# Kernel optimization log

Hardware: AMD Instinct MI355X
Metric: run time of the kernel (lower is better)

## Reference

```python
import jax, jax.numpy as jnp
import numpy as np

B, T, D, H = 2, 2048, 2048, 16
HD = D // H  # 128


def _rope_tables(t, hd):
    # standard RoPE frequencies
    inv_freq = 1.0 / (10000.0 ** (np.arange(0, hd, 2, dtype=np.float32) / hd))
    pos = np.arange(t, dtype=np.float32)
    freqs = np.outer(pos, inv_freq)          # [t, hd/2]
    emb = np.concatenate([freqs, freqs], -1)  # [t, hd]
    return jnp.asarray(np.cos(emb)), jnp.asarray(np.sin(emb))


def setup_inputs() -> dict:
    key = jax.random.key(0)
    k1, k2, k3 = jax.random.split(key, 3)
    x = jax.random.normal(k1, (B, T, D), dtype=jnp.float32)
    cos, sin = _rope_tables(T, HD)
    Wqkv = jax.random.normal(k2, (3 * D, D), dtype=jnp.float32) * (D ** -0.5)
    Wout = jax.random.normal(k3, (D, D), dtype=jnp.float32) * (D ** -0.5)
    return {"x": x, "cos": cos, "sin": sin, "Wqkv": Wqkv, "Wout": Wout}


def _rotate_half(u):
    u1, u2 = jnp.split(u, 2, axis=-1)
    return jnp.concatenate([-u2, u1], axis=-1)


def _apply_rotary(u, cos, sin):
    # u: [b,h,t,hd]; cos/sin: [t,hd] broadcast over b,h
    return u * cos[None, None] + _rotate_half(u) * sin[None, None]


def reference(x, cos, sin, Wqkv, Wout):
    b, t, d = x.shape
    qkv = jnp.einsum('btd,ed->bte', x, Wqkv)                 # [b,t,3d]
    qkv = qkv.reshape(b, t, 3, H, HD).transpose(2, 0, 3, 1, 4)  # [3,b,h,t,hd]
    q, k, v = qkv[0], qkv[1], qkv[2]
    q = _apply_rotary(q, cos, sin)
    k = _apply_rotary(k, cos, sin)
    scale = 1.0 / jnp.sqrt(jnp.asarray(HD, dtype=x.dtype))
    scores = jnp.einsum('bhqe,bhke->bhqk', q, k) * scale      # [b,h,t,t]
    causal = jnp.tril(jnp.ones((t, t), dtype=bool))
    scores = jnp.where(causal[None, None], scores, jnp.asarray(-jnp.inf, dtype=scores.dtype))
    probs = jax.nn.softmax(scores, axis=-1)
    attn = jnp.einsum('bhqk,bhke->bhqe', probs, v)            # [b,h,t,hd]
    attn = attn.transpose(0, 2, 1, 3).reshape(b, t, d)
    return jnp.einsum('btd,ed->bte', attn, Wout)
```

## Files before the change

### kernel.cpp

```cpp
#include <hip/hip_runtime.h>
#include <hip/hip_bf16.h>
#include <stdint.h>

#define T_SEQ 2048
#define D_MODEL 2048
#define N_HEADS 16
#define HEAD_DIM 128

typedef __hip_bfloat16 bf16_t;
typedef __attribute__((ext_vector_type(8))) short short8;
typedef __attribute__((ext_vector_type(4))) short short4v;
typedef __attribute__((ext_vector_type(4))) float f32x4;

__device__ __forceinline__ unsigned short f2bf(float x) {
  union { float f; unsigned u; } c; c.f = x;
  unsigned u = c.u;
  u += 0x7fffu + ((u >> 16) & 1u);
  return (unsigned short)(u >> 16);
}
__device__ __forceinline__ float bf2f(short v) {
  union { unsigned u; float f; } c;
  c.u = ((unsigned)(unsigned short)v) << 16;
  return c.f;
}
__device__ __forceinline__ void async16(const bf16_t* g, bf16_t* l) {
  __builtin_amdgcn_global_load_lds(
      (const __attribute__((address_space(1))) void*)g,
      (__attribute__((address_space(3))) void*)l, 16, 0, 0);
}

__global__ __launch_bounds__(256) void cvt_kernel(const float* __restrict__ in,
                                                  unsigned short* __restrict__ out,
                                                  int n4) {
  int i = blockIdx.x * 256 + threadIdx.x;
  if (i >= n4) return;
  float4 v = ((const float4*)in)[i];
  short4v o;
  o[0] = (short)f2bf(v.x); o[1] = (short)f2bf(v.y);
  o[2] = (short)f2bf(v.z); o[3] = (short)f2bf(v.w);
  ((short4v*)out)[i] = o;
}

template<int F32OUT>
__global__ __launch_bounds__(512, 4) void gemm_tp_kernel(
    const bf16_t* __restrict__ A, const bf16_t* __restrict__ Bm,
    float* __restrict__ Cf, unsigned short* __restrict__ Cb,
    int M, int N, int K, int nbn) {
  __shared__ bf16_t lds[36864];
  const int tid = threadIdx.x;
  const int w = tid >> 6, lane = tid & 63;
  const int wm = w >> 2, wn = w & 3;
  const int l15 = lane & 15, g = lane >> 4;

  const int nwg = gridDim.x;
  const int cpx = nwg >> 3;
  const int wg = (blockIdx.x & 7) * cpx + (blockIdx.x >> 3);
  const int bm0 = (wg / nbn) * 128, bn0 = (wg % nbn) * 256;

  const int sl = tid >> 3;
  const int su = (tid & 7) ^ (sl & 7);
  const int srow = (sl << 1) | (su >> 2);
  const int sc8 = su & 3;
  const bf16_t* agA = A + (size_t)(bm0 + srow) * K + sc8 * 8;
  const bf16_t* agB = Bm + (size_t)(bn0 + srow) * K + sc8 * 8;

#define STAGE(KT, SB) do {                                                    \
    bf16_t* _d = lds + (SB) * 12288 + w * 512;         \
    async16(agA + (size_t)(KT) * 32, _d);                                     \
    async16(agB + (size_t)(KT) * 32, _d + 4096);                              \
    async16(agB + 128 * (size_t)K + (size_t)(KT) * 32, _d + 8192);            \
  } while (0)

  const int lhalf = l15 >> 1;
  const int aoff = lhalf * 64 + (((((l15 & 1) << 2) | g) ^ lhalf)) * 8;
  const bf16_t* Abase = lds + wm * 2048 + aoff;
  const bf16_t* Bbase = lds + 4096 + wn * 2048 + aoff;

  f32x4 acc[4][4];
#pragma unroll
  for (int i = 0; i < 4; ++i)
#pragma unroll
    for (int j = 0; j < 4; ++j)
#pragma unroll
      for (int e = 0; e < 4; ++e) acc[i][j][e] = 0.0f;

  STAGE(0, 0);
  STAGE(1, 1);

  const int NT = K >> 5;
  int cb = 0, sb = 2;
  for (int kt = 0; kt < NT - 1; ++kt) {
    asm volatile("s_waitcnt vmcnt(3)" ::: "memory");
    __builtin_amdgcn_s_barrier();
    const bf16_t* Ab = Abase + cb * 12288;
    const bf16_t* Bb = Bbase + cb * 12288;
    short8 af[4], bfr[4];
#pragma unroll
    for (int mi = 0; mi < 4; ++mi) af[mi] = *(const short8*)(Ab + mi * 512);
#pragma unroll
    for (int ni = 0; ni < 4; ++ni) bfr[ni] = *(const short8*)(Bb + ni * 512);
    if (kt < NT - 2) STAGE(kt + 2, sb);
    __builtin_amdgcn_s_setprio(1);
#pragma unroll
    for (int mi = 0; mi < 4; ++mi)
#pragma unroll
      for (int ni = 0; ni < 4; ++ni)
        acc[mi][ni] = __builtin_amdgcn_mfma_f32_16x16x32_bf16(
            af[mi], bfr[ni], acc[mi][ni], 0, 0, 0);
    __builtin_amdgcn_s_setprio(0);
    cb = (cb == 2) ? 0 : cb + 1;
    sb = (sb == 2) ? 0 : sb + 1;
  }
  {
    asm volatile("s_waitcnt vmcnt(0)" ::: "memory");
    __builtin_amdgcn_s_barrier();
    const bf16_t* Ab = Abase + cb * 12288;
    const bf16_t* Bb = Bbase + cb * 12288;
    short8 af[4], bfr[4];
#pragma unroll
    for (int mi = 0; mi < 4; ++mi) af[mi] = *(const short8*)(Ab + mi * 512);
#pragma unroll
    for (int ni = 0; ni < 4; ++ni) bfr[ni] = *(const short8*)(Bb + ni * 512);
    __builtin_amdgcn_s_setprio(1);
#pragma unroll
    for (int mi = 0; mi < 4; ++mi)
#pragma unroll
      for (int ni = 0; ni < 4; ++ni)
        acc[mi][ni] = __builtin_amdgcn_mfma_f32_16x16x32_bf16(
            af[mi], bfr[ni], acc[mi][ni], 0, 0, 0);
    __builtin_amdgcn_s_setprio(0);
  }
#undef STAGE

#pragma unroll
  for (int mi = 0; mi < 4; ++mi)
#pragma unroll
    for (int ni = 0; ni < 4; ++ni)
#pragma unroll
      for (int r = 0; r < 4; ++r) {
        int mr = bm0 + wm * 64 + mi * 16 + g * 4 + r;
        int nc = bn0 + wn * 64 + ni * 16 + l15;
        if (F32OUT)
          Cf[(size_t)mr * N + nc] = acc[mi][ni][r];
        else
          Cb[(size_t)mr * N + nc] = f2bf(acc[mi][ni][r]);
      }
}

__global__ __launch_bounds__(256) void rope_kernel(
    const bf16_t* __restrict__ qkv,
    const float* __restrict__ cosb, const float* __restrict__ sinb,
    bf16_t* __restrict__ qo, bf16_t* __restrict__ ko, bf16_t* __restrict__ vT) {
  const int nTT = T_SEQ / 64;
  const int bx = blockIdx.x;
  const int bh = bx / nTT, tt = bx % nTT;
  const int b = bh / N_HEADS, h = bh % N_HEADS;
  const int tid = threadIdx.x;
  __shared__ bf16_t vlds[64][136];

  const float SC = 0.08838834764831845f;

#pragma unroll
  for (int it = 0; it < 2; ++it) {
    int item = it * 256 + tid;
    int r = item >> 3, cg = item & 7;
    int t = tt * 64 + r;
    int c0 = cg * 8;
    size_t base = ((size_t)b * T_SEQ + t) * (size_t)(3 * D_MODEL) + (size_t)h * HEAD_DIM;

    float cs0[8], sn0[8], cs1[8], sn1[8];
    {
      const float* cp = cosb + (size_t)t * HEAD_DIM + c0;
      const float* sp = sinb + (size_t)t * HEAD_DIM + c0;
      float4 a0 = *(const float4*)(cp), a1 = *(const float4*)(cp + 4);
      float4 b0 = *(const float4*)(cp + 64), b1 = *(const float4*)(cp + 68);
      float4 s0 = *(const float4*)(sp), s1 = *(const float4*)(sp + 4);
      float4 t0 = *(const float4*)(sp + 64), t1 = *(const float4*)(sp + 68);
      cs0[0]=a0.x; cs0[1]=a0.y; cs0[2]=a0.z; cs0[3]=a0.w; cs0[4]=a1.x; cs0[5]=a1.y; cs0[6]=a1.z; cs0[7]=a1.w;
      cs1[0]=b0.x; cs1[1]=b0.y; cs1[2]=b0.z; cs1[3]=b0.w; cs1[4]=b1.x; cs1[5]=b1.y; cs1[6]=b1.z; cs1[7]=b1.w;
      sn0[0]=s0.x; sn0[1]=s0.y; sn0[2]=s0.z; sn0[3]=s0.w; sn0[4]=s1.x; sn0[5]=s1.y; sn0[6]=s1.z; sn0[7]=s1.w;
      sn1[0]=t0.x; sn1[1]=t0.y; sn1[2]=t0.z; sn1[3]=t0.w; sn1[4]=t1.x; sn1[5]=t1.y; sn1[6]=t1.z; sn1[7]=t1.w;
    }

#pragma unroll
    for (int sec = 0; sec < 2; ++sec) {
      size_t sbase = base + (size_t)sec * D_MODEL;
      short8 lo = *(const short8*)(qkv + sbase + c0);
      short8 hi = *(const short8*)(qkv + sbase + 64 + c0);
      short8 olo, ohi;
#pragma unroll
      for (int e = 0; e < 8; ++e) {
        float xl = bf2f(lo[e]), xh = bf2f(hi[e]);
        float rl = xl * cs0[e] - xh * sn0[e];
        float rh = xh * cs1[e] + xl * sn1[e];
        if (sec == 0) { rl *= SC; rh *= SC; }
        olo[e] = (short)f2bf(rl);
        ohi[e] = (short)f2bf(rh);
      }
      bf16_t* dst = (sec == 0 ? qo : ko) + ((size_t)bh * T_SEQ + t) * HEAD_DIM + c0;
      *(short8*)dst = olo;
      *(short8*)(dst + 64) = ohi;
    }

    short8 v0 = *(const short8*)(qkv + base + 2 * D_MODEL + c0);
    short8 v1 = *(const short8*)(qkv + base + 2 * D_MODEL + 64 + c0);
    *(short8*)&vlds[r][c0] = v0;
    *(short8*)&vlds[r][64 + c0] = v1;
  }
  __syncthreads();

  int hd = tid >> 1, hf = tid & 1;
  bf16_t* dst = vT + ((size_t)bh * HEAD_DIM + hd) * T_SEQ + tt * 64 + hf * 32;
#pragma unroll
  for (int jj = 0; jj < 4; ++jj) {
    short8 o;
#pragma unroll
    for (int e = 0; e < 8; ++e)
      o[e] = *(const short*)&vlds[hf * 32 + jj * 8 + e][hd];
    *(short8*)(dst + jj * 8) = o;
  }
}

__global__ __launch_bounds__(256) void attn_kernel(
    const bf16_t* __restrict__ q, const bf16_t* __restrict__ k,
    const bf16_t* __restrict__ vT, unsigned short* __restrict__ attn) {
  const int bx = blockIdx.x;
  const int bh = bx & 31;
  const int qt = 31 - (bx >> 5);
  const int b = bh / N_HEADS, h = bh % N_HEADS;
  const int tid = threadIdx.x;
  const int w = tid >> 6, lane = tid & 63;
  const int l15 = lane & 15, g = lane >> 4;
  const float LOG2E = 1.44269504088896340736f;

  __shared__ bf16_t Ks[2][64 * 128];
  __shared__ bf16_t Vs[2][128 * 64];
  __shared__ bf16_t plds[4][16][72];

  const bf16_t* qb = q + (size_t)bh * T_SEQ * HEAD_DIM;
  const bf16_t* kb = k + (size_t)bh * T_SEQ * HEAD_DIM;
  const bf16_t* vb = vT + (size_t)bh * HEAD_DIM * T_SEQ;

  const int qrow = qt * 64 + w * 16 + l15;
  short8 qf[4];
#pragma unroll
  for (int kk = 0; kk < 4; ++kk)
    qf[kk] = *(const short8*)(qb + (size_t)qrow * HEAD_DIM + kk * 32 + g * 8);

  float m[4], l[4];
  f32x4 acc[8];
#pragma unroll
  for (int r = 0; r < 4; ++r) { m[r] = -3.0e38f; l[r] = 0.0f; }
#pragma unroll
  for (int fh = 0; fh < 8; ++fh)
#pragma unroll
    for (int e = 0; e < 4; ++e) acc[fh][e] = 0.0f;

#define STAGE_TILES(KT, BU)                                                      \
  {                                                                              \
    _Pragma("unroll")                                                            \
    for (int j = 0; j < 4; ++j) {                                                \
      int s = j * 4 + w;                                                         \
      int row = s * 4 + (lane >> 4);                                             \
      int gc = (lane & 15) ^ (row & 7);                                          \
      async16(kb + (size_t)((KT) * 64 + row) * HEAD_DIM + gc * 8,                \
              &Ks[BU][s * 512]);                                                 \
    }                                                                            \
    _Pragma("unroll")                                                            \
    for (int j = 0; j < 4; ++j) {                                                \
      int s = j * 4 + w;                                                         \
      int row = s * 8 + (lane >> 3);                                             \
      int gc = (lane & 7) ^ (row & 7);                                           \
      async16(vb + (size_t)row * T_SEQ + (KT) * 64 + gc * 8,                     \
              &Vs[BU][s * 512]);                                                 \
    }                                                                            \
  }

  STAGE_TILES(0, 0);
  __syncthreads();
  int buf = 0;

  for (int kt = 0; kt <= qt; ++kt) {
    if (kt < qt) STAGE_TILES(kt + 1, buf ^ 1);

    f32x4 s[4];
#pragma unroll
    for (int f = 0; f < 4; ++f)
#pragma unroll
      for (int e = 0; e < 4; ++e) s[f][e] = 0.0f;
    __builtin_amdgcn_s_setprio(1);
#pragma unroll
    for (int f = 0; f < 4; ++f) {
      int row = f * 16 + l15;
      int r7 = l15 & 7;
#pragma unroll
      for (int kk = 0; kk < 4; ++kk) {
        short8 kf = *(const short8*)(&Ks[buf][row * 128 + (((kk * 4 + g) ^ r7) << 3)]);
        s[f] = __builtin_amdgcn_mfma_f32_16x16x32_bf16(qf[kk], kf, s[f], 0, 0, 0);
      }
    }
    __builtin_amdgcn_s_setprio(0);

    if (kt == qt) {
#pragma unroll
      for (int f = 0; f < 4; ++f) {
        int kv = f * 16 + l15;
#pragma unroll
        for (int r = 0; r < 4; ++r) {
          int qq = w * 16 + g * 4 + r;
          if (kv > qq) s[f][r] = -3.0e38f;
        }
      }
    }
    float rmax[4];
#pragma unroll
    for (int r = 0; r < 4; ++r)
      rmax[r] = fmaxf(fmaxf(s[0][r], s[1][r]), fmaxf(s[2][r], s[3][r]));
#pragma unroll
    for (int off = 1; off < 16; off <<= 1)
#pragma unroll
      for (int r = 0; r < 4; ++r)
        rmax[r] = fmaxf(rmax[r], __shfl_xor(rmax[r], off, 64));

    float fac[4], rsum[4];
#pragma unroll
    for (int r = 0; r < 4; ++r) {
      float mn = fmaxf(m[r], rmax[r]);
      fac[r] = exp2f((m[r] - mn) * LOG2E);
      m[r] = mn;
      rsum[r] = 0.0f;
    }
#pragma unroll
    for (int f = 0; f < 4; ++f)
#pragma unroll
      for (int r = 0; r < 4; ++r) {
        float pv = exp2f((s[f][r] - m[r]) * LOG2E);
        s[f][r] = pv;
        rsum[r] += pv;
      }
#pragma unroll
    for (int off = 1; off < 16; off <<= 1)
#pragma unroll
      for (int r = 0; r < 4; ++r)
        rsum[r] += __shfl_xor(rsum[r], off, 64);
#pragma unroll
    for (int r = 0; r < 4; ++r) l[r] = l[r] * fac[r] + rsum[r];
#pragma unroll
    for (int fh = 0; fh < 8; ++fh)
#pragma unroll
      for (int r = 0; r < 4; ++r) acc[fh][r] *= fac[r];

#pragma unroll
    for (int f = 0; f < 4; ++f)
#pragma unroll
      for (int r = 0; r < 4; ++r)
        *(unsigned short*)&plds[w][g * 4 + r][f * 16 + l15] = f2bf(s[f][r]);

    short8 pf0 = *(const short8*)&plds[w][l15][g * 8];
    short8 pf1 = *(const short8*)&plds[w][l15][32 + g * 8];

    __builtin_amdgcn_s_setprio(1);
#pragma unroll
    for (int fh = 0; fh < 8; ++fh) {
      int row = fh * 16 + l15;
      int r7 = l15 & 7;
      short8 vf0 = *(const short8*)(&Vs[buf][row * 64 + ((g ^ r7) << 3)]);
      short8 vf1 = *(const short8*)(&Vs[buf][row * 64 + (((4 + g) ^ r7) << 3)]);
      acc[fh] = __builtin_amdgcn_mfma_f32_16x16x32_bf16(pf0, vf0, acc[fh], 0, 0, 0);
      acc[fh] = __builtin_amdgcn_mfma_f32_16x16x32_bf16(pf1, vf1, acc[fh], 0, 0, 0);
    }
    __builtin_amdgcn_s_setprio(0);

    __syncthreads();
    buf ^= 1;
  }

  float inv[4];
#pragma unroll
  for (int r = 0; r < 4; ++r) inv[r] = 1.0f / l[r];
#pragma unroll
  for (int fh = 0; fh < 8; ++fh)
#pragma unroll
    for (int r = 0; r < 4; ++r) {
      int tg = qt * 64 + w * 16 + g * 4 + r;
      attn[((size_t)b * T_SEQ + tg) * D_MODEL + (size_t)h * HEAD_DIM + fh * 16 + l15] =
          f2bf(acc[fh][r] * inv[r]);
    }
}

extern "C" void kernel_launch(void* const* d_in, const int* in_sizes, int n_in,
                              void* d_out, int out_size, void* d_ws, size_t ws_size,
                              hipStream_t stream) {
  const float* x    = (const float*)d_in[0];
  const float* cosb = (const float*)d_in[1];
  const float* sinb = (const float*)d_in[2];
  const float* Wqkv = (const float*)d_in[3];
  const float* Wout = (const float*)d_in[4];
  float* out = (float*)d_out;

  char* ws = (char*)d_ws;
  size_t off = 0;
  bf16_t* xb    = (bf16_t*)(ws + off); off += (size_t)4096 * 2048 * 2;
  bf16_t* wqkvb = (bf16_t*)(ws + off); off += (size_t)6144 * 2048 * 2;
  bf16_t* woutb = (bf16_t*)(ws + off); off += (size_t)2048 * 2048 * 2;
  bf16_t* qkvb  = (bf16_t*)(ws + off); off += (size_t)4096 * 6144 * 2;
  bf16_t* qb    = (bf16_t*)(ws + off); off += (size_t)32 * 2048 * 128 * 2;
  bf16_t* kb    = (bf16_t*)(ws + off); off += (size_t)32 * 2048 * 128 * 2;
  bf16_t* vTb   = (bf16_t*)(ws + off); off += (size_t)32 * 2048 * 128 * 2;
  bf16_t* attnb = xb;

  cvt_kernel<<<8192, 256, 0, stream>>>(x, (unsigned short*)xb, 4096 * 2048 / 4);
  cvt_kernel<<<12288, 256, 0, stream>>>(Wqkv, (unsigned short*)wqkvb, 6144 * 2048 / 4);
  cvt_kernel<<<4096, 256, 0, stream>>>(Wout, (unsigned short*)woutb, 2048 * 2048 / 4);

  gemm_tp_kernel<0><<<768, 512, 0, stream>>>(xb, wqkvb, nullptr, (unsigned short*)qkvb,
                                             4096, 6144, 2048, 24);

  rope_kernel<<<1024, 256, 0, stream>>>(qkvb, cosb, sinb, qb, kb, vTb);

  attn_kernel<<<1024, 256, 0, stream>>>(qb, kb, vTb, (unsigned short*)attnb);

  gemm_tp_kernel<1><<<256, 512, 0, stream>>>(attnb, woutb, out, nullptr,
                                             4096, 2048, 2048, 8);
}
```

Baseline: 297.7 us.

## Software-pipeline attention loop: overlap next QK^T with current softmax and PV

Restructures the flash-attention inner loop so K and V tiles are staged separately. The QK^T MFMAs for the next tile are issued before the softmax and PV of the current tile, with explicit vmcnt waits and raw s_barriers in place of __syncthreads. The goal is to hide softmax and exp latency behind matrix work and to load K one tile ahead of V. This adds register pressure from the second score buffer, and the hand-tuned waitcnt counts must exactly match the number of outstanding async loads.

```diff
diff --git a/kernel.cpp b/kernel.cpp
--- a/kernel.cpp
+++ b/kernel.cpp
@@ -65,7 +65,7 @@
   const bf16_t* agB = Bm + (size_t)(bn0 + srow) * K + sc8 * 8;
 
 #define STAGE(KT, SB) do {                                                    \
-    bf16_t* _d = lds + (SB) * 12288 + w * 512;         \
+    bf16_t* _d = lds + (SB) * 12288 + w * 512;                                \
     async16(agA + (size_t)(KT) * 32, _d);                                     \
     async16(agB + (size_t)(KT) * 32, _d + 4096);                              \
     async16(agB + 128 * (size_t)K + (size_t)(KT) * 32, _d + 8192);            \
@@ -256,8 +256,10 @@
 #pragma unroll
     for (int e = 0; e < 4; ++e) acc[fh][e] = 0.0f;
 
-#define STAGE_TILES(KT, BU)                                                      \
-  {                                                                              \
+  f32x4 SA[4], SB[4];
+  const int r7 = l15 & 7;
+
+#define STAGE_K(KT, BU) {                                                        \
     _Pragma("unroll")                                                            \
     for (int j = 0; j < 4; ++j) {                                                \
       int s = j * 4 + w;                                                         \
@@ -266,6 +268,8 @@
       async16(kb + (size_t)((KT) * 64 + row) * HEAD_DIM + gc * 8,                \
               &Ks[BU][s * 512]);                                                 \
     }                                                                            \
+  }
+#define STAGE_V(KT, BU) {                                                        \
     _Pragma("unroll")                                                            \
     for (int j = 0; j < 4; ++j) {                                                \
       int s = j * 4 + w;                                                         \
@@ -276,104 +280,135 @@
     }                                                                            \
   }
 
-  STAGE_TILES(0, 0);
-  __syncthreads();
-  int buf = 0;
-
-  for (int kt = 0; kt <= qt; ++kt) {
-    if (kt < qt) STAGE_TILES(kt + 1, buf ^ 1);
-
-    f32x4 s[4];
-#pragma unroll
-    for (int f = 0; f < 4; ++f)
-#pragma unroll
-      for (int e = 0; e < 4; ++e) s[f][e] = 0.0f;
-    __builtin_amdgcn_s_setprio(1);
-#pragma unroll
-    for (int f = 0; f < 4; ++f) {
-      int row = f * 16 + l15;
-      int r7 = l15 & 7;
-#pragma unroll
-      for (int kk = 0; kk < 4; ++kk) {
-        short8 kf = *(const short8*)(&Ks[buf][row * 128 + (((kk * 4 + g) ^ r7) << 3)]);
-        s[f] = __builtin_amdgcn_mfma_f32_16x16x32_bf16(qf[kk], kf, s[f], 0, 0, 0);
-      }
-    }
-    __builtin_amdgcn_s_setprio(0);
-
-    if (kt == qt) {
-#pragma unroll
-      for (int f = 0; f < 4; ++f) {
-        int kv = f * 16 + l15;
-#pragma unroll
-        for (int r = 0; r < 4; ++r) {
-          int qq = w * 16 + g * 4 + r;
-          if (kv > qq) s[f][r] = -3.0e38f;
-        }
-      }
-    }
-    float rmax[4];
-#pragma unroll
-    for (int r = 0; r < 4; ++r)
-      rmax[r] = fmaxf(fmaxf(s[0][r], s[1][r]), fmaxf(s[2][r], s[3][r]));
-#pragma unroll
-    for (int off = 1; off < 16; off <<= 1)
-#pragma unroll
-      for (int r = 0; r < 4; ++r)
-        rmax[r] = fmaxf(rmax[r], __shfl_xor(rmax[r], off, 64));
-
-    float fac[4], rsum[4];
-#pragma unroll
-    for (int r = 0; r < 4; ++r) {
-      float mn = fmaxf(m[r], rmax[r]);
-      fac[r] = exp2f((m[r] - mn) * LOG2E);
-      m[r] = mn;
-      rsum[r] = 0.0f;
-    }
-#pragma unroll
-    for (int f = 0; f < 4; ++f)
-#pragma unroll
-      for (int r = 0; r < 4; ++r) {
-        float pv = exp2f((s[f][r] - m[r]) * LOG2E);
-        s[f][r] = pv;
-        rsum[r] += pv;
-      }
-#pragma unroll
-    for (int off = 1; off < 16; off <<= 1)
-#pragma unroll
-      for (int r = 0; r < 4; ++r)
-        rsum[r] += __shfl_xor(rsum[r], off, 64);
-#pragma unroll
-    for (int r = 0; r < 4; ++r) l[r] = l[r] * fac[r] + rsum[r];
-#pragma unroll
-    for (int fh = 0; fh < 8; ++fh)
-#pragma unroll
-      for (int r = 0; r < 4; ++r) acc[fh][r] *= fac[r];
-
-#pragma unroll
-    for (int f = 0; f < 4; ++f)
-#pragma unroll
-      for (int r = 0; r < 4; ++r)
-        *(unsigned short*)&plds[w][g * 4 + r][f * 16 + l15] = f2bf(s[f][r]);
-
-    short8 pf0 = *(const short8*)&plds[w][l15][g * 8];
-    short8 pf1 = *(const short8*)&plds[w][l15][32 + g * 8];
-
-    __builtin_amdgcn_s_setprio(1);
-#pragma unroll
-    for (int fh = 0; fh < 8; ++fh) {
-      int row = fh * 16 + l15;
-      int r7 = l15 & 7;
-      short8 vf0 = *(const short8*)(&Vs[buf][row * 64 + ((g ^ r7) << 3)]);
-      short8 vf1 = *(const short8*)(&Vs[buf][row * 64 + (((4 + g) ^ r7) << 3)]);
-      acc[fh] = __builtin_amdgcn_mfma_f32_16x16x32_bf16(pf0, vf0, acc[fh], 0, 0, 0);
-      acc[fh] = __builtin_amdgcn_mfma_f32_16x16x32_bf16(pf1, vf1, acc[fh], 0, 0, 0);
-    }
-    __builtin_amdgcn_s_setprio(0);
-
-    __syncthreads();
-    buf ^= 1;
-  }
+#define QK(SX, BU, DIAG) do {                                                    \
+    _Pragma("unroll")                                                            \
+    for (int f = 0; f < 4; ++f)                                                  \
+      _Pragma("unroll")                                                          \
+      for (int e = 0; e < 4; ++e) SX[f][e] = 0.0f;                               \
+    __builtin_amdgcn_s_setprio(1);                                               \
+    _Pragma("unroll")                                                            \
+    for (int f = 0; f < 4; ++f) {                                                \
+      int row = f * 16 + l15;                                                    \
+      _Pragma("unroll")                                                          \
+      for (int kk = 0; kk < 4; ++kk) {                                           \
+        short8 kf = *(const short8*)(&Ks[BU][row * 128 + (((kk * 4 + g) ^ r7) << 3)]); \
+        SX[f] = __builtin_amdgcn_mfma_f32_16x16x32_bf16(qf[kk], kf, SX[f], 0, 0, 0); \
+      }                                                                          \
+    }                                                                            \
+    __builtin_amdgcn_s_setprio(0);                                               \
+    if (DIAG) {                                                                  \
+      _Pragma("unroll")                                                          \
+      for (int f = 0; f < 4; ++f) {                                              \
+        int kv = f * 16 + l15;                                                   \
+        _Pragma("unroll")                                                        \
+        for (int r = 0; r < 4; ++r) {                                            \
+          int qq = w * 16 + g * 4 + r;                                           \
+          if (kv > qq) SX[f][r] = -3.0e38f;                                      \
+        }                                                                        \
+      }                                                                          \
+    }                                                                            \
+  } while (0)
+
+#define SOFTMAX_PV(SX, VBU) do {                                                 \
+    float rmax[4];                                                               \
+    _Pragma("unroll")                                                            \
+    for (int r = 0; r < 4; ++r)                                                  \
+      rmax[r] = fmaxf(fmaxf(SX[0][r], SX[1][r]), fmaxf(SX[2][r], SX[3][r]));     \
+    _Pragma("unroll")                                                            \
+    for (int off = 1; off < 16; off <<= 1)                                       \
+      _Pragma("unroll")                                                          \
+      for (int r = 0; r < 4; ++r)                                                \
+        rmax[r] = fmaxf(rmax[r], __shfl_xor(rmax[r], off, 64));                  \
+    float fac[4], rsum[4];                                                       \
+    _Pragma("unroll")                                                            \
+    for (int r = 0; r < 4; ++r) {                                                \
+      float mn = fmaxf(m[r], rmax[r]);                                           \
+      fac[r] = exp2f((m[r] - mn) * LOG2E);                                       \
+      m[r] = mn;                                                                 \
+      rsum[r] = 0.0f;                                                            \
+    }                                                                            \
+    _Pragma("unroll")                                                            \
+    for (int f = 0; f < 4; ++f)                                                  \
+      _Pragma("unroll")                                                          \
+      for (int r = 0; r < 4; ++r) {                                              \
+        float pv = exp2f((SX[f][r] - m[r]) * LOG2E);                             \
+        SX[f][r] = pv;                                                           \
+        rsum[r] += pv;                                                           \
+      }                                                                          \
+    _Pragma("unroll")                                                            \
+    for (int off = 1; off < 16; off <<= 1)                                       \
+      _Pragma("unroll")                                                          \
+      for (int r = 0; r < 4; ++r)                                                \
+        rsum[r] += __shfl_xor(rsum[r], off, 64);                                 \
+    _Pragma("unroll")                                                            \
+    for (int r = 0; r < 4; ++r) l[r] = l[r] * fac[r] + rsum[r];                  \
+    _Pragma("unroll")                                                            \
+    for (int fh = 0; fh < 8; ++fh)                                               \
+      _Pragma("unroll")                                                          \
+      for (int r = 0; r < 4; ++r) acc[fh][r] *= fac[r];                          \
+    _Pragma("unroll")                                                            \
+    for (int f = 0; f < 4; ++f)                                                  \
+      _Pragma("unroll")                                                          \
+      for (int r = 0; r < 4; ++r)                                                \
+        *(unsigned short*)&plds[w][g * 4 + r][f * 16 + l15] = f2bf(SX[f][r]);    \
+    short8 pf0 = *(const short8*)&plds[w][l15][g * 8];                           \
+    short8 pf1 = *(const short8*)&plds[w][l15][32 + g * 8];                      \
+    __builtin_amdgcn_s_setprio(1);                                               \
+    _Pragma("unroll")                                                            \
+    for (int fh = 0; fh < 8; ++fh) {                                             \
+      int row = fh * 16 + l15;                                                   \
+      short8 vf0 = *(const short8*)(&Vs[VBU][row * 64 + ((g ^ r7) << 3)]);       \
+      short8 vf1 = *(const short8*)(&Vs[VBU][row * 64 + (((4 + g) ^ r7) << 3)]); \
+      acc[fh] = __builtin_amdgcn_mfma_f32_16x16x32_bf16(pf0, vf0, acc[fh], 0, 0, 0); \
+      acc[fh] = __builtin_amdgcn_mfma_f32_16x16x32_bf16(pf1, vf1, acc[fh], 0, 0, 0); \
+    }                                                                            \
+    __builtin_amdgcn_s_setprio(0);                                               \
+  } while (0)
+
+  STAGE_K(0, 0);
+  STAGE_V(0, 0);
+  if (qt >= 1) {
+    STAGE_K(1, 1);
+    asm volatile("s_waitcnt vmcnt(8)" ::: "memory");
+  } else {
+    asm volatile("s_waitcnt vmcnt(4)" ::: "memory");
+  }
+  __builtin_amdgcn_s_barrier();
+  QK(SA, 0, qt == 0);
+  __builtin_amdgcn_s_barrier();
+
+  for (int kt = 0; kt < qt - 1; ++kt) {
+    STAGE_K(kt + 2, kt & 1);
+    STAGE_V(kt + 1, (kt + 1) & 1);
+    asm volatile("s_waitcnt vmcnt(8)" ::: "memory");
+    __builtin_amdgcn_s_barrier();
+    QK(SB, (kt + 1) & 1, false);
+    SOFTMAX_PV(SA, kt & 1);
+#pragma unroll
+    for (int f = 0; f < 4; ++f) SA[f] = SB[f];
+    __builtin_amdgcn_s_barrier();
+  }
+
+  if (qt >= 1) {
+    int kt = qt - 1;
+    STAGE_V(qt, qt & 1);
+    asm volatile("s_waitcnt vmcnt(4)" ::: "memory");
+    __builtin_amdgcn_s_barrier();
+    QK(SB, qt & 1, true);
+    SOFTMAX_PV(SA, kt & 1);
+#pragma unroll
+    for (int f = 0; f < 4; ++f) SA[f] = SB[f];
+    __builtin_amdgcn_s_barrier();
+  }
+
+  asm volatile("s_waitcnt vmcnt(0)" ::: "memory");
+  __builtin_amdgcn_s_barrier();
+  SOFTMAX_PV(SA, qt & 1);
+
+#undef STAGE_K
+#undef STAGE_V
+#undef QK
+#undef SOFTMAX_PV
 
   float inv[4];
 #pragma unroll
```

Result: no change. 295.1 us (-0.8%).

## Process two 64-row query tiles per attention block to reuse K/V tiles

Applied to the files above, without the earlier changes.

Each attention workgroup now handles 128 query rows as two 64-row sub-tiles that share every staged K and V tile. The grid is halved, and a tail iteration handles the diagonal tile of the second sub-tile. This is meant to halve K/V global-to-LDS traffic per query row and raise MFMA work per sync. In exchange each wave holds roughly twice the registers, and launch_bounds(256,2) may force spills. Load balancing across the causal triangle also gets coarser.

```diff
diff --git a/kernel.cpp b/kernel.cpp
--- a/kernel.cpp
+++ b/kernel.cpp
@@ -65,7 +65,7 @@
   const bf16_t* agB = Bm + (size_t)(bn0 + srow) * K + sc8 * 8;
 
 #define STAGE(KT, SB) do {                                                    \
-    bf16_t* _d = lds + (SB) * 12288 + w * 512;         \
+    bf16_t* _d = lds + (SB) * 12288 + w * 512;                                \
     async16(agA + (size_t)(KT) * 32, _d);                                     \
     async16(agB + (size_t)(KT) * 32, _d + 4096);                              \
     async16(agB + 128 * (size_t)K + (size_t)(KT) * 32, _d + 8192);            \
@@ -221,16 +221,17 @@
   }
 }
 
-__global__ __launch_bounds__(256) void attn_kernel(
+__global__ __launch_bounds__(256, 2) void attn_kernel(
     const bf16_t* __restrict__ q, const bf16_t* __restrict__ k,
     const bf16_t* __restrict__ vT, unsigned short* __restrict__ attn) {
   const int bx = blockIdx.x;
   const int bh = bx & 31;
-  const int qt = 31 - (bx >> 5);
+  const int qt = 15 - (bx >> 5);
   const int b = bh / N_HEADS, h = bh % N_HEADS;
   const int tid = threadIdx.x;
   const int w = tid >> 6, lane = tid & 63;
   const int l15 = lane & 15, g = lane >> 4;
+  const int r7 = l15 & 7;
   const float LOG2E = 1.44269504088896340736f;
 
   __shared__ bf16_t Ks[2][64 * 128];
@@ -241,20 +242,22 @@
   const bf16_t* kb = k + (size_t)bh * T_SEQ * HEAD_DIM;
   const bf16_t* vb = vT + (size_t)bh * HEAD_DIM * T_SEQ;
 
-  const int qrow = qt * 64 + w * 16 + l15;
-  short8 qf[4];
-#pragma unroll
-  for (int kk = 0; kk < 4; ++kk)
-    qf[kk] = *(const short8*)(qb + (size_t)qrow * HEAD_DIM + kk * 32 + g * 8);
-
-  float m[4], l[4];
-  f32x4 acc[8];
-#pragma unroll
-  for (int r = 0; r < 4; ++r) { m[r] = -3.0e38f; l[r] = 0.0f; }
+  const int qr0 = qt * 128 + w * 16 + l15;
+  short8 qf0[4], qf1[4];
+#pragma unroll
+  for (int kk = 0; kk < 4; ++kk) {
+    qf0[kk] = *(const short8*)(qb + (size_t)qr0 * HEAD_DIM + kk * 32 + g * 8);
+    qf1[kk] = *(const short8*)(qb + (size_t)(qr0 + 64) * HEAD_DIM + kk * 32 + g * 8);
+  }
+
+  float m0[4], l0[4], m1[4], l1[4];
+  f32x4 acc0[8], acc1[8];
+#pragma unroll
+  for (int r = 0; r < 4; ++r) { m0[r] = -3.0e38f; l0[r] = 0.0f; m1[r] = -3.0e38f; l1[r] = 0.0f; }
 #pragma unroll
   for (int fh = 0; fh < 8; ++fh)
 #pragma unroll
-    for (int e = 0; e < 4; ++e) acc[fh][e] = 0.0f;
+    for (int e = 0; e < 4; ++e) { acc0[fh][e] = 0.0f; acc1[fh][e] = 0.0f; }
 
 #define STAGE_TILES(KT, BU)                                                      \
   {                                                                              \
@@ -276,115 +279,150 @@
     }                                                                            \
   }
 
+#define SMPV(SX, MM, LL, ACC, VBU) do {                                          \
+    float rmax[4];                                                               \
+    _Pragma("unroll")                                                            \
+    for (int r = 0; r < 4; ++r)                                                  \
+      rmax[r] = fmaxf(fmaxf(SX[0][r], SX[1][r]), fmaxf(SX[2][r], SX[3][r]));     \
+    _Pragma("unroll")                                                            \
+    for (int off = 1; off < 16; off <<= 1)                                       \
+      _Pragma("unroll")                                                          \
+      for (int r = 0; r < 4; ++r)                                                \
+        rmax[r] = fmaxf(rmax[r], __shfl_xor(rmax[r], off, 64));                  \
+    float fac[4], rsum[4];                                                       \
+    _Pragma("unroll")                                                            \
+    for (int r = 0; r < 4; ++r) {                                                \
+      float mn = fmaxf(MM[r], rmax[r]);                                          \
+      fac[r] = exp2f((MM[r] - mn) * LOG2E);                                      \
+      MM[r] = mn;                                                                \
+      rsum[r] = 0.0f;                                                            \
+    }                                                                            \
+    _Pragma("unroll")                                                            \
+    for (int f = 0; f < 4; ++f)                                                  \
+      _Pragma("unroll")                                                          \
+      for (int r = 0; r < 4; ++r) {                                              \
+        float pv = exp2f((SX[f][r] - MM[r]) * LOG2E);                            \
+        SX[f][r] = pv;                                                           \
+        rsum[r] += pv;                                                           \
+      }                                                                          \
+    _Pragma("unroll")                                                            \
+    for (int off = 1; off < 16; off <<= 1)                                       \
+      _Pragma("unroll")                                                          \
+      for (int r = 0; r < 4; ++r)                                                \
+        rsum[r] += __shfl_xor(rsum[r], off, 64);                                 \
+    _Pragma("unroll")                                                            \
+    for (int r = 0; r < 4; ++r) LL[r] = LL[r] * fac[r] + rsum[r];                \
+    _Pragma("unroll")                                                            \
+    for (int fh = 0; fh < 8; ++fh)                                               \
+      _Pragma("unroll")                                                          \
+      for (int r = 0; r < 4; ++r) ACC[fh][r] *= fac[r];                          \
+    _Pragma("unroll")                                                            \
+    for (int f = 0; f < 4; ++f)                                                  \
+      _Pragma("unroll")                                                          \
+      for (int r = 0; r < 4; ++r)                                                \
+        *(unsigned short*)&plds[w][g * 4 + r][f * 16 + l15] = f2bf(SX[f][r]);    \
+    short8 pf0 = *(const short8*)&plds[w][l15][g * 8];                           \
+    short8 pf1 = *(const short8*)&plds[w][l15][32 + g * 8];                      \
+    __builtin_amdgcn_s_setprio(1);                                               \
+    _Pragma("unroll")                                                            \
+    for (int fh = 0; fh < 8; ++fh) {                                             \
+      int row = fh * 16 + l15;                                                   \
+      short8 vf0 = *(const short8*)(&Vs[VBU][row * 64 + ((g ^ r7) << 3)]);       \
+      short8 vf1 = *(const short8*)(&Vs[VBU][row * 64 + (((4 + g) ^ r7) << 3)]); \
+      ACC[fh] = __builtin_amdgcn_mfma_f32_16x16x32_bf16(pf0, vf0, ACC[fh], 0, 0, 0); \
+      ACC[fh] = __builtin_amdgcn_mfma_f32_16x16x32_bf16(pf1, vf1, ACC[fh], 0, 0, 0); \
+    }                                                                            \
+    __builtin_amdgcn_s_setprio(0);                                               \
+  } while (0)
+
   STAGE_TILES(0, 0);
   __syncthreads();
   int buf = 0;
-
-  for (int kt = 0; kt <= qt; ++kt) {
-    if (kt < qt) STAGE_TILES(kt + 1, buf ^ 1);
-
-    f32x4 s[4];
+  const int lastk = 2 * qt;
+
+  for (int kt = 0; kt <= lastk; ++kt) {
+    STAGE_TILES(kt + 1, buf ^ 1);
+
+    f32x4 S0[4], S1[4];
 #pragma unroll
     for (int f = 0; f < 4; ++f)
 #pragma unroll
-      for (int e = 0; e < 4; ++e) s[f][e] = 0.0f;
+      for (int e = 0; e < 4; ++e) { S0[f][e] = 0.0f; S1[f][e] = 0.0f; }
     __builtin_amdgcn_s_setprio(1);
 #pragma unroll
     for (int f = 0; f < 4; ++f) {
       int row = f * 16 + l15;
-      int r7 = l15 & 7;
 #pragma unroll
       for (int kk = 0; kk < 4; ++kk) {
         short8 kf = *(const short8*)(&Ks[buf][row * 128 + (((kk * 4 + g) ^ r7) << 3)]);
-        s[f] = __builtin_amdgcn_mfma_f32_16x16x32_bf16(qf[kk], kf, s[f], 0, 0, 0);
+        S0[f] = __builtin_amdgcn_mfma_f32_16x16x32_bf16(qf0[kk], kf, S0[f], 0, 0, 0);
+        S1[f] = __builtin_amdgcn_mfma_f32_16x16x32_bf16(qf1[kk], kf, S1[f], 0, 0, 0);
       }
     }
     __builtin_amdgcn_s_setprio(0);
 
-    if (kt == qt) {
+    if (kt == lastk) {
 #pragma unroll
       for (int f = 0; f < 4; ++f) {
         int kv = f * 16 + l15;
 #pragma unroll
         for (int r = 0; r < 4; ++r) {
           int qq = w * 16 + g * 4 + r;
-          if (kv > qq) s[f][r] = -3.0e38f;
+          if (kv > qq) S0[f][r] = -3.0e38f;
         }
       }
     }
-    float rmax[4];
-#pragma unroll
-    for (int r = 0; r < 4; ++r)
-      rmax[r] = fmaxf(fmaxf(s[0][r], s[1][r]), fmaxf(s[2][r], s[3][r]));
-#pragma unroll
-    for (int off = 1; off < 16; off <<= 1)
-#pragma unroll
-      for (int r = 0; r < 4; ++r)
-        rmax[r] = fmaxf(rmax[r], __shfl_xor(rmax[r], off, 64));
-
-    float fac[4], rsum[4];
-#pragma unroll
-    for (int r = 0; r < 4; ++r) {
-      float mn = fmaxf(m[r], rmax[r]);
-      fac[r] = exp2f((m[r] - mn) * LOG2E);
-      m[r] = mn;
-      rsum[r] = 0.0f;
-    }
-#pragma unroll
-    for (int f = 0; f < 4; ++f)
-#pragma unroll
-      for (int r = 0; r < 4; ++r) {
-        float pv = exp2f((s[f][r] - m[r]) * LOG2E);
-        s[f][r] = pv;
-        rsum[r] += pv;
-      }
-#pragma unroll
-    for (int off = 1; off < 16; off <<= 1)
-#pragma unroll
-      for (int r = 0; r < 4; ++r)
-        rsum[r] += __shfl_xor(rsum[r], off, 64);
-#pragma unroll
-    for (int r = 0; r < 4; ++r) l[r] = l[r] * fac[r] + rsum[r];
-#pragma unroll
-    for (int fh = 0; fh < 8; ++fh)
-#pragma unroll
-      for (int r = 0; r < 4; ++r) acc[fh][r] *= fac[r];
-
-#pragma unroll
-    for (int f = 0; f < 4; ++f)
-#pragma unroll
-      for (int r = 0; r < 4; ++r)
-        *(unsigned short*)&plds[w][g * 4 + r][f * 16 + l15] = f2bf(s[f][r]);
-
-    short8 pf0 = *(const short8*)&plds[w][l15][g * 8];
-    short8 pf1 = *(const short8*)&plds[w][l15][32 + g * 8];
-
-    __builtin_amdgcn_s_setprio(1);
-#pragma unroll
-    for (int fh = 0; fh < 8; ++fh) {
-      int row = fh * 16 + l15;
-      int r7 = l15 & 7;
-      short8 vf0 = *(const short8*)(&Vs[buf][row * 64 + ((g ^ r7) << 3)]);
-      short8 vf1 = *(const short8*)(&Vs[buf][row * 64 + (((4 + g) ^ r7) << 3)]);
-      acc[fh] = __builtin_amdgcn_mfma_f32_16x16x32_bf16(pf0, vf0, acc[fh], 0, 0, 0);
-      acc[fh] = __builtin_amdgcn_mfma_f32_16x16x32_bf16(pf1, vf1, acc[fh], 0, 0, 0);
-    }
-    __builtin_amdgcn_s_setprio(0);
+
+    SMPV(S0, m0, l0, acc0, buf);
+    SMPV(S1, m1, l1, acc1, buf);
 
     __syncthreads();
     buf ^= 1;
   }
 
-  float inv[4];
-#pragma unroll
-  for (int r = 0; r < 4; ++r) inv[r] = 1.0f / l[r];
+  {
+    f32x4 S1[4];
+#pragma unroll
+    for (int f = 0; f < 4; ++f)
+#pragma unroll
+      for (int e = 0; e < 4; ++e) S1[f][e] = 0.0f;
+    __builtin_amdgcn_s_setprio(1);
+#pragma unroll
+    for (int f = 0; f < 4; ++f) {
+      int row = f * 16 + l15;
+#pragma unroll
+      for (int kk = 0; kk < 4; ++kk) {
+        short8 kf = *(const short8*)(&Ks[buf][row * 128 + (((kk * 4 + g) ^ r7) << 3)]);
+        S1[f] = __builtin_amdgcn_mfma_f32_16x16x32_bf16(qf1[kk], kf, S1[f], 0, 0, 0);
+      }
+    }
+    __builtin_amdgcn_s_setprio(0);
+#pragma unroll
+    for (int f = 0; f < 4; ++f) {
+      int kv = f * 16 + l15;
+#pragma unroll
+      for (int r = 0; r < 4; ++r) {
+        int qq = w * 16 + g * 4 + r;
+        if (kv > qq) S1[f][r] = -3.0e38f;
+      }
+    }
+    SMPV(S1, m1, l1, acc1, buf);
+  }
+
+#undef STAGE_TILES
+#undef SMPV
+
+  float inv0[4], inv1[4];
+#pragma unroll
+  for (int r = 0; r < 4; ++r) { inv0[r] = 1.0f / l0[r]; inv1[r] = 1.0f / l1[r]; }
 #pragma unroll
   for (int fh = 0; fh < 8; ++fh)
 #pragma unroll
     for (int r = 0; r < 4; ++r) {
-      int tg = qt * 64 + w * 16 + g * 4 + r;
-      attn[((size_t)b * T_SEQ + tg) * D_MODEL + (size_t)h * HEAD_DIM + fh * 16 + l15] =
-          f2bf(acc[fh][r] * inv[r]);
+      int tg0 = qt * 128 + w * 16 + g * 4 + r;
+      size_t col = (size_t)h * HEAD_DIM + fh * 16 + l15;
+      attn[((size_t)b * T_SEQ + tg0) * D_MODEL + col] = f2bf(acc0[fh][r] * inv0[r]);
+      attn[((size_t)b * T_SEQ + tg0 + 64) * D_MODEL + col] = f2bf(acc1[fh][r] * inv1[r]);
     }
 }
 
@@ -418,7 +456,7 @@
 
   rope_kernel<<<1024, 256, 0, stream>>>(qkvb, cosb, sinb, qb, kb, vTb);
 
-  attn_kernel<<<1024, 256, 0, stream>>>(qb, kb, vTb, (unsigned short*)attnb);
+  attn_kernel<<<512, 256, 0, stream>>>(qb, kb, vTb, (unsigned short*)attnb);
 
   gemm_tp_kernel<1><<<256, 512, 0, stream>>>(attnb, woutb, out, nullptr,
                                              4096, 2048, 2048, 8);
```

Result: slower. 316.7 us (+6.4%).

## Single-buffer V tile with split K/V barriers and raise attention occupancy

Applied to the files above, without the earlier changes.

The attention kernel now keeps a single V buffer in shared memory while K stays double-buffered. Each iteration issues the V load for the current tile and the K prefetch for the next tile, then waits on the V load only just before the PV matmul using vmcnt-based barriers. Together with launch_bounds(256,2), the smaller LDS footprint is meant to allow two workgroups per CU. The cost is that the current V load is now exposed within the iteration, and the manual waitcnt counting relies on the exact number of outstanding loads.

```diff
diff --git a/kernel.cpp b/kernel.cpp
--- a/kernel.cpp
+++ b/kernel.cpp
@@ -65,7 +65,7 @@
   const bf16_t* agB = Bm + (size_t)(bn0 + srow) * K + sc8 * 8;
 
 #define STAGE(KT, SB) do {                                                    \
-    bf16_t* _d = lds + (SB) * 12288 + w * 512;         \
+    bf16_t* _d = lds + (SB) * 12288 + w * 512;                                \
     async16(agA + (size_t)(KT) * 32, _d);                                     \
     async16(agB + (size_t)(KT) * 32, _d + 4096);                              \
     async16(agB + 128 * (size_t)K + (size_t)(KT) * 32, _d + 8192);            \
@@ -221,7 +221,7 @@
   }
 }
 
-__global__ __launch_bounds__(256) void attn_kernel(
+__global__ __launch_bounds__(256, 2) void attn_kernel(
     const bf16_t* __restrict__ q, const bf16_t* __restrict__ k,
     const bf16_t* __restrict__ vT, unsigned short* __restrict__ attn) {
   const int bx = blockIdx.x;
@@ -231,10 +231,11 @@
   const int tid = threadIdx.x;
   const int w = tid >> 6, lane = tid & 63;
   const int l15 = lane & 15, g = lane >> 4;
+  const int r7 = l15 & 7;
   const float LOG2E = 1.44269504088896340736f;
 
   __shared__ bf16_t Ks[2][64 * 128];
-  __shared__ bf16_t Vs[2][128 * 64];
+  __shared__ bf16_t Vs[128 * 64];
   __shared__ bf16_t plds[4][16][72];
 
   const bf16_t* qb = q + (size_t)bh * T_SEQ * HEAD_DIM;
@@ -256,8 +257,7 @@
 #pragma unroll
     for (int e = 0; e < 4; ++e) acc[fh][e] = 0.0f;
 
-#define STAGE_TILES(KT, BU)                                                      \
-  {                                                                              \
+#define STAGE_K(KT, BU) {                                                        \
     _Pragma("unroll")                                                            \
     for (int j = 0; j < 4; ++j) {                                                \
       int s = j * 4 + w;                                                         \
@@ -266,22 +266,27 @@
       async16(kb + (size_t)((KT) * 64 + row) * HEAD_DIM + gc * 8,                \
               &Ks[BU][s * 512]);                                                 \
     }                                                                            \
+  }
+#define STAGE_V(KT) {                                                            \
     _Pragma("unroll")                                                            \
     for (int j = 0; j < 4; ++j) {                                                \
       int s = j * 4 + w;                                                         \
       int row = s * 8 + (lane >> 3);                                             \
       int gc = (lane & 7) ^ (row & 7);                                           \
       async16(vb + (size_t)row * T_SEQ + (KT) * 64 + gc * 8,                     \
-              &Vs[BU][s * 512]);                                                 \
+              &Vs[s * 512]);                                                     \
     }                                                                            \
   }
 
-  STAGE_TILES(0, 0);
-  __syncthreads();
-  int buf = 0;
+  STAGE_K(0, 0);
 
   for (int kt = 0; kt <= qt; ++kt) {
-    if (kt < qt) STAGE_TILES(kt + 1, buf ^ 1);
+    const int kbuf = kt & 1;
+    asm volatile("s_waitcnt vmcnt(0)" ::: "memory");
+    __builtin_amdgcn_s_barrier();
+
+    STAGE_V(kt);
+    if (kt < qt) STAGE_K(kt + 1, kbuf ^ 1);
 
     f32x4 s[4];
 #pragma unroll
@@ -292,10 +297,9 @@
 #pragma unroll
     for (int f = 0; f < 4; ++f) {
       int row = f * 16 + l15;
-      int r7 = l15 & 7;
 #pragma unroll
       for (int kk = 0; kk < 4; ++kk) {
-        short8 kf = *(const short8*)(&Ks[buf][row * 128 + (((kk * 4 + g) ^ r7) << 3)]);
+        short8 kf = *(const short8*)(&Ks[kbuf][row * 128 + (((kk * 4 + g) ^ r7) << 3)]);
         s[f] = __builtin_amdgcn_mfma_f32_16x16x32_bf16(qf[kk], kf, s[f], 0, 0, 0);
       }
     }
@@ -312,6 +316,7 @@
         }
       }
     }
+
     float rmax[4];
 #pragma unroll
     for (int r = 0; r < 4; ++r)
@@ -359,21 +364,27 @@
     short8 pf0 = *(const short8*)&plds[w][l15][g * 8];
     short8 pf1 = *(const short8*)&plds[w][l15][32 + g * 8];
 
+    if (kt < qt) {
+      asm volatile("s_waitcnt vmcnt(4)" ::: "memory");
+    } else {
+      asm volatile("s_waitcnt vmcnt(0)" ::: "memory");
+    }
+    __builtin_amdgcn_s_barrier();
+
     __builtin_amdgcn_s_setprio(1);
 #pragma unroll
     for (int fh = 0; fh < 8; ++fh) {
       int row = fh * 16 + l15;
-      int r7 = l15 & 7;
-      short8 vf0 = *(const short8*)(&Vs[buf][row * 64 + ((g ^ r7) << 3)]);
-      short8 vf1 = *(const short8*)(&Vs[buf][row * 64 + (((4 + g) ^ r7) << 3)]);
+      short8 vf0 = *(const short8*)(&Vs[row * 64 + ((g ^ r7) << 3)]);
+      short8 vf1 = *(const short8*)(&Vs[row * 64 + (((4 + g) ^ r7) << 3)]);
       acc[fh] = __builtin_amdgcn_mfma_f32_16x16x32_bf16(pf0, vf0, acc[fh], 0, 0, 0);
       acc[fh] = __builtin_amdgcn_mfma_f32_16x16x32_bf16(pf1, vf1, acc[fh], 0, 0, 0);
     }
     __builtin_amdgcn_s_setprio(0);
-
-    __syncthreads();
-    buf ^= 1;
-  }
+  }
+
+#undef STAGE_K
+#undef STAGE_V
 
   float inv[4];
 #pragma unroll
```

Result: no change. 294.9 us (-0.9%).
